# Kernel tuning notes

Measured on AMD Instinct MI355X. Metric: run time of the kernel, lower is better.

## Reference

```python
import jax, jax.numpy as jnp
import numpy as np

N = 500_000   # nodes
D = 256       # feature dim
S = 20_000    # segments (pooled outputs)


def setup_inputs() -> dict:
    key = jax.random.key(0)
    ks = jax.random.split(key, 6)
    x = jax.random.normal(ks[0], (N, D), dtype=jnp.float32)
    # weights must be strictly positive (raised to a learned power)
    weights = jax.random.uniform(ks[1], (N, 1), dtype=jnp.float32) + 0.01
    Wg = jax.random.normal(ks[2], (D, 1), dtype=jnp.float32) / np.sqrt(D)
    bg = jnp.zeros((1,), dtype=jnp.float32)
    Wm = jax.random.normal(ks[3], (D, D), dtype=jnp.float32) / np.sqrt(D)
    bm = jnp.zeros((D,), dtype=jnp.float32)
    p = jax.random.normal(ks[4], (1,), dtype=jnp.float32)
    index = jnp.sort(jax.random.randint(ks[5], (N,), 0, S, dtype=jnp.int32))
    return {"x": x, "weights": weights, "Wg": Wg, "bg": bg, "Wm": Wm,
            "bm": bm, "p": p, "index": index, "num_segments": S}


def reference(x, weights, Wg, bg, Wm, bm, p, index, num_segments):
    # gate_nn: per-node attention logit [N, 1]
    gate = x @ Wg + bg
    # segment-wise max subtraction for numerical stability
    seg_max = jax.ops.segment_max(gate, index, num_segments=num_segments)
    gate = gate - seg_max[index]
    # weighted exponential: weights ** pow * exp(gate)
    gate = (weights ** p) * jnp.exp(gate)
    # segment-wise normalization (softmax denominator)
    denom = jax.ops.segment_sum(gate, index, num_segments=num_segments)
    gate = gate / (denom[index] + 1e-10)
    # message_nn: per-node messages [N, D]
    msg = x @ Wm + bm
    # attention-weighted segment sum -> [S, D]
    return jax.ops.segment_sum(gate * msg, index, num_segments=num_segments)
```

## Files before the change

### kernel.cpp

```cpp
#include <hip/hip_runtime.h>
#include <math.h>

#define DDIM 256
#define CHUNK 512
#define WCHUNK 128
#define TM 64
#define TN 64
#define TK 32

__global__ __launch_bounds__(256) void k_fused(
    const float* __restrict__ x, const float* __restrict__ weights,
    const float* __restrict__ Wg, const float* __restrict__ bg,
    const float* __restrict__ p_, const int* __restrict__ index,
    float* __restrict__ pooled, float* __restrict__ denom, int N)
{
    __shared__ int   s_seg[CHUNK];
    __shared__ float s_wp[CHUNK];
    const int n0 = blockIdx.x * CHUNK;
    const float p = p_[0];
    for (int jj = threadIdx.x; jj < CHUNK; jj += 256) {
        int i = n0 + jj;
        if (i < N) {
            s_seg[jj] = index[i];
            s_wp[jj]  = powf(weights[i], p);
        } else {
            s_seg[jj] = -1;
        }
    }
    __syncthreads();

    const int lane = threadIdx.x & 63;
    const int wave = threadIdx.x >> 6;
    const float4 wg = ((const float4*)Wg)[lane];
    const float b = bg[0];
    const int j0 = wave * WCHUNK;
    const float4* x4 = (const float4*)x;

    float4 acc = make_float4(0.f, 0.f, 0.f, 0.f);
    float wsum = 0.f;
    int prev = -1;

    for (int j = j0; j < j0 + WCHUNK; ++j) {
        int i = n0 + j;
        if (i >= N) break;
        int s = s_seg[j];
        if (s != prev) {
            if (prev >= 0) {
                float* pp = &pooled[(size_t)prev * DDIM + lane * 4];
                atomicAdd(pp + 0, acc.x); atomicAdd(pp + 1, acc.y);
                atomicAdd(pp + 2, acc.z); atomicAdd(pp + 3, acc.w);
                if (lane == 0) atomicAdd(&denom[prev], wsum);
            }
            acc = make_float4(0.f, 0.f, 0.f, 0.f);
            wsum = 0.f;
            prev = s;
        }
        float4 xv = x4[(size_t)i * (DDIM/4) + lane];
        float d = xv.x*wg.x + xv.y*wg.y + xv.z*wg.z + xv.w*wg.w;
        #pragma unroll
        for (int m = 32; m >= 1; m >>= 1) d += __shfl_xor(d, m, 64);
        float w = s_wp[j] * __expf(d + b);
        acc.x += w * xv.x; acc.y += w * xv.y;
        acc.z += w * xv.z; acc.w += w * xv.w;
        wsum += w;
    }
    if (prev >= 0) {
        float* pp = &pooled[(size_t)prev * DDIM + lane * 4];
        atomicAdd(pp + 0, acc.x); atomicAdd(pp + 1, acc.y);
        atomicAdd(pp + 2, acc.z); atomicAdd(pp + 3, acc.w);
        if (lane == 0) atomicAdd(&denom[prev], wsum);
    }
}

__global__ __launch_bounds__(256) void k_gemm(
    const float* __restrict__ pooled, const float* __restrict__ Wm,
    const float* __restrict__ bm, const float* __restrict__ denom,
    float* __restrict__ out, int S)
{
    __shared__ float At[TK][TM + 4];
    __shared__ float Bs[TK][TN];
    const int tx = threadIdx.x & 15;
    const int ty = threadIdx.x >> 4;
    const int r0 = blockIdx.x * TM;
    const int c0 = blockIdx.y * TN;
    float acc[4][4] = {};

    for (int k0 = 0; k0 < DDIM; k0 += TK) {
        #pragma unroll
        for (int it = 0; it < 2; ++it) {
            int idx = threadIdx.x + it * 256;
            {
                int r  = idx >> 3;
                int kq = (idx & 7) * 4;
                float4 a = make_float4(0.f, 0.f, 0.f, 0.f);
                if (r0 + r < S)
                    a = *(const float4*)&pooled[(size_t)(r0 + r) * DDIM + k0 + kq];
                At[kq + 0][r] = a.x; At[kq + 1][r] = a.y;
                At[kq + 2][r] = a.z; At[kq + 3][r] = a.w;
            }
            {
                int k  = idx >> 4;
                int cq = (idx & 15) * 4;
                *(float4*)&Bs[k][cq] =
                    *(const float4*)&Wm[(size_t)(k0 + k) * DDIM + c0 + cq];
            }
        }
        __syncthreads();
        #pragma unroll
        for (int k = 0; k < TK; ++k) {
            const float4 av = *(const float4*)&At[k][ty * 4];
            const float4 bv = *(const float4*)&Bs[k][tx * 4];
            float a4[4] = {av.x, av.y, av.z, av.w};
            float b4[4] = {bv.x, bv.y, bv.z, bv.w};
            #pragma unroll
            for (int i = 0; i < 4; ++i)
                #pragma unroll
                for (int j = 0; j < 4; ++j)
                    acc[i][j] += a4[i] * b4[j];
        }
        __syncthreads();
    }

    const float4 bmv = *(const float4*)&bm[c0 + tx * 4];
    #pragma unroll
    for (int i = 0; i < 4; ++i) {
        int row = r0 + ty * 4 + i;
        if (row >= S) continue;
        float dn = denom[row];
        float scale = 1.f / (dn + 1e-10f);
        float gs = dn * scale;
        float4 o;
        o.x = acc[i][0] * scale + gs * bmv.x;
        o.y = acc[i][1] * scale + gs * bmv.y;
        o.z = acc[i][2] * scale + gs * bmv.z;
        o.w = acc[i][3] * scale + gs * bmv.w;
        *(float4*)&out[(size_t)row * DDIM + c0 + tx * 4] = o;
    }
}

extern "C" void kernel_launch(void* const* d_in, const int* in_sizes, int n_in,
                              void* d_out, int out_size, void* d_ws, size_t ws_size,
                              hipStream_t stream) {
    const float* x       = (const float*)d_in[0];
    const float* weights = (const float*)d_in[1];
    const float* Wg      = (const float*)d_in[2];
    const float* bg      = (const float*)d_in[3];
    const float* Wm      = (const float*)d_in[4];
    const float* bm      = (const float*)d_in[5];
    const float* p       = (const float*)d_in[6];
    const int*   index   = (const int*)d_in[7];

    const int N = in_sizes[1];
    const int D = in_sizes[2];
    const int S = out_size / D;
    float* out = (float*)d_out;

    float* denom  = (float*)d_ws;
    float* pooled = denom + S;

    hipMemsetAsync(denom,  0, (size_t)S * sizeof(float), stream);
    hipMemsetAsync(pooled, 0, (size_t)S * D * sizeof(float), stream);

    k_fused<<<(N + CHUNK - 1) / CHUNK, 256, 0, stream>>>(
        x, weights, Wg, bg, p, index, pooled, denom, N);

    dim3 g2((S + TM - 1) / TM, D / TN);
    k_gemm<<<g2, 256, 0, stream>>>(pooled, Wm, bm, denom, out, S);
}
```

Measured before the change: 746.9 us.

## Batch four row loads per wave, halve chunk size, merge memsets

The fused gating/pooling kernel now issues four x-row loads per wave before reducing, and interleaves the four shuffle reductions so memory and cross-lane latency overlap. The chunk is halved to 256 nodes, which doubles the block count and shortens each wave's serial loop, at the cost of more boundary atomics. The two workspace memsets are combined into one contiguous memset. Out-of-range rows are clamped on load and skipped by checking the segment sentinel.

```diff
diff --git a/kernel.cpp b/kernel.cpp
--- a/kernel.cpp
+++ b/kernel.cpp
@@ -2,8 +2,8 @@
 #include <math.h>
 
 #define DDIM 256
-#define CHUNK 512
-#define WCHUNK 128
+#define CHUNK 256
+#define WCHUNK 64
 #define TM 64
 #define TN 64
 #define TK 32
@@ -18,7 +18,8 @@
     __shared__ float s_wp[CHUNK];
     const int n0 = blockIdx.x * CHUNK;
     const float p = p_[0];
-    for (int jj = threadIdx.x; jj < CHUNK; jj += 256) {
+    {
+        int jj = threadIdx.x;
         int i = n0 + jj;
         if (i < N) {
             s_seg[jj] = index[i];
@@ -40,29 +41,49 @@
     float wsum = 0.f;
     int prev = -1;
 
-    for (int j = j0; j < j0 + WCHUNK; ++j) {
-        int i = n0 + j;
-        if (i >= N) break;
-        int s = s_seg[j];
-        if (s != prev) {
-            if (prev >= 0) {
-                float* pp = &pooled[(size_t)prev * DDIM + lane * 4];
-                atomicAdd(pp + 0, acc.x); atomicAdd(pp + 1, acc.y);
-                atomicAdd(pp + 2, acc.z); atomicAdd(pp + 3, acc.w);
-                if (lane == 0) atomicAdd(&denom[prev], wsum);
+    for (int j = j0; j < j0 + WCHUNK; j += 4) {
+        if (n0 + j >= N) break;
+
+        float4 xv[4];
+        #pragma unroll
+        for (int t = 0; t < 4; ++t) {
+            int i = n0 + j + t;
+            int ic = i < N ? i : N - 1;
+            xv[t] = x4[(size_t)ic * (DDIM/4) + lane];
+        }
+
+        float d[4];
+        #pragma unroll
+        for (int t = 0; t < 4; ++t)
+            d[t] = xv[t].x*wg.x + xv[t].y*wg.y + xv[t].z*wg.z + xv[t].w*wg.w;
+
+        #pragma unroll
+        for (int m = 32; m >= 1; m >>= 1) {
+            #pragma unroll
+            for (int t = 0; t < 4; ++t)
+                d[t] += __shfl_xor(d[t], m, 64);
+        }
+
+        #pragma unroll
+        for (int t = 0; t < 4; ++t) {
+            int s = s_seg[j + t];
+            if (s < 0) break;
+            if (s != prev) {
+                if (prev >= 0) {
+                    float* pp = &pooled[(size_t)prev * DDIM + lane * 4];
+                    atomicAdd(pp + 0, acc.x); atomicAdd(pp + 1, acc.y);
+                    atomicAdd(pp + 2, acc.z); atomicAdd(pp + 3, acc.w);
+                    if (lane == 0) atomicAdd(&denom[prev], wsum);
+                }
+                acc = make_float4(0.f, 0.f, 0.f, 0.f);
+                wsum = 0.f;
+                prev = s;
             }
-            acc = make_float4(0.f, 0.f, 0.f, 0.f);
-            wsum = 0.f;
-            prev = s;
+            float w = s_wp[j + t] * __expf(d[t] + b);
+            acc.x += w * xv[t].x; acc.y += w * xv[t].y;
+            acc.z += w * xv[t].z; acc.w += w * xv[t].w;
+            wsum += w;
         }
-        float4 xv = x4[(size_t)i * (DDIM/4) + lane];
-        float d = xv.x*wg.x + xv.y*wg.y + xv.z*wg.z + xv.w*wg.w;
-        #pragma unroll
-        for (int m = 32; m >= 1; m >>= 1) d += __shfl_xor(d, m, 64);
-        float w = s_wp[j] * __expf(d + b);
-        acc.x += w * xv.x; acc.y += w * xv.y;
-        acc.z += w * xv.z; acc.w += w * xv.w;
-        wsum += w;
     }
     if (prev >= 0) {
         float* pp = &pooled[(size_t)prev * DDIM + lane * 4];
@@ -158,8 +179,7 @@
     float* denom  = (float*)d_ws;
     float* pooled = denom + S;
 
-    hipMemsetAsync(denom,  0, (size_t)S * sizeof(float), stream);
-    hipMemsetAsync(pooled, 0, (size_t)S * D * sizeof(float), stream);
+    hipMemsetAsync(denom, 0, (size_t)S * (D + 1) * sizeof(float), stream);
 
     k_fused<<<(N + CHUNK - 1) / CHUNK, 256, 0, stream>>>(
         x, weights, Wg, bg, p, index, pooled, denom, N);
```

Result: no change. 735.9 us (-1.5%).
